# Kernel optimization log

Measured on AMD Instinct MI355X. Metric: run time of the kernel, lower is better.

## Reference

```python
import jax, jax.numpy as jnp
import numpy as np

EPS = 1e-5

def _layernorm(x, w, b):
    mu = jnp.mean(x, axis=-1, keepdims=True)
    var = jnp.mean((x - mu) ** 2, axis=-1, keepdims=True)
    return (x - mu) * jax.lax.rsqrt(var + EPS) * w + b

def _ssm(x, in_proj_w, x_proj_w, dt_proj_w, dt_proj_b, conv1d_w, conv1d_b,
         A_log, D, out_proj_w, norm_w, norm_b, d_state=16):
    # x: (B, L, d_model)
    xz = jnp.einsum('bld,ed->ble', x, in_proj_w)          # (B,L,2*d_inner)
    d_inner = xz.shape[-1] // 2
    x_in, z = xz[..., :d_inner], xz[..., d_inner:]
    # depthwise conv1d, kernel 3, pad 1
    xc = jax.lax.conv_general_dilated(
        jnp.transpose(x_in, (0, 2, 1)), conv1d_w,
        window_strides=(1,), padding=((1, 1),),
        feature_group_count=d_inner,
        dimension_numbers=('NCH', 'OIH', 'NCH'))
    xc = jnp.transpose(xc, (0, 2, 1)) + conv1d_b          # (B,L,d_inner)
    xc = jax.nn.silu(xc)
    dbc = jnp.einsum('bld,ed->ble', xc, x_proj_w)         # (B,L,1+2*d_state)
    delta = dbc[..., :1]
    B_mat = dbc[..., 1:1 + d_state]
    C_mat = dbc[..., 1 + d_state:]
    delta = jax.nn.softplus(jnp.einsum('blo,eo->ble', delta, dt_proj_w) + dt_proj_b)  # (B,L,d_inner)
    A = -jnp.exp(A_log)                                   # (d_inner,d_state)
    dA = jnp.exp(delta[..., None] * A[None, None])        # (B,L,d_inner,d_state)
    xbu = delta[..., None] * B_mat[:, :, None, :] * xc[..., None]
    def combine(c1, c2):
        a1, b1 = c1
        a2, b2 = c2
        return (a2 * a1, b2 + a2 * b1)
    _, h = jax.lax.associative_scan(combine, (dA, xbu), axis=1)  # h_t = dA_t h_{t-1} + xbu_t, h_0=0
    y = jnp.sum(h * C_mat[:, :, None, :], axis=-1)        # (B,L,d_inner)
    y = y + xc * D
    y = y * jax.nn.silu(z)
    y = _layernorm(y, norm_w, norm_b)
    return jnp.einsum('ble,de->bld', y, out_proj_w)

def reference(x, in_proj_w, x_proj_w, dt_proj_w, dt_proj_b, conv1d_w, conv1d_b,
              A_log, D, out_proj_w, norm_ssm_w, norm_ssm_b, norm1_w, norm1_b,
              dw_w, dw_b, gate):
    B, C, H, W = x.shape
    # local branch: depthwise 7x7 conv
    local = jax.lax.conv_general_dilated(
        x, dw_w, window_strides=(1, 1), padding=((3, 3), (3, 3)),
        feature_group_count=C, dimension_numbers=('NCHW', 'OIHW', 'NCHW'))
    local = local + dw_b[None, :, None, None]
    L = H * W
    max_seq_len = 256
    if L <= max_seq_len:
        x_flat = jnp.transpose(x, (0, 2, 3, 1)).reshape(B, L, C)
        ssm_out = _ssm(_layernorm(x_flat, norm1_w, norm1_b), in_proj_w, x_proj_w,
                       dt_proj_w, dt_proj_b, conv1d_w, conv1d_b, A_log, D,
                       out_proj_w, norm_ssm_w, norm_ssm_b)
        ssm_out = jnp.transpose(ssm_out.reshape(B, H, W, C), (0, 3, 1, 2))
    else:
        scale = (max_seq_len / L) ** 0.5
        h_s = max(1, int(H * scale))
        w_s = max(1, int(W * scale))
        # adaptive avg pool; H,W chosen divisible by h_s,w_s -> exact block mean
        x_small = x.reshape(B, C, h_s, H // h_s, w_s, W // w_s).mean(axis=(3, 5))
        x_flat = jnp.transpose(x_small, (0, 2, 3, 1)).reshape(B, h_s * w_s, C)
        ssm_small = _ssm(_layernorm(x_flat, norm1_w, norm1_b), in_proj_w, x_proj_w,
                         dt_proj_w, dt_proj_b, conv1d_w, conv1d_b, A_log, D,
                         out_proj_w, norm_ssm_w, norm_ssm_b)
        ssm_small = jnp.transpose(ssm_small.reshape(B, h_s, w_s, C), (0, 3, 1, 2))
        ssm_out = jax.image.resize(ssm_small, (B, C, H, W), method='bilinear')  # align_corners=False
    g = jax.nn.sigmoid(gate[0])
    return x + g * ssm_out + (1.0 - g) * local

def setup_inputs() -> dict:
    key = jax.random.key(0)
    ks = jax.random.split(key, 8)
    C, d_state, d_inner = 192, 16, 384
    Bsz, H, W = 32, 64, 64
    s = 0.02
    A = jnp.broadcast_to(jnp.arange(1, d_state + 1, dtype=jnp.float32), (d_inner, d_state))
    return {
        'x': jax.random.normal(ks[0], (Bsz, C, H, W), jnp.float32),
        'in_proj_w': jax.random.normal(ks[1], (2 * d_inner, C), jnp.float32) * s,
        'x_proj_w': jax.random.normal(ks[2], (2 * d_state + 1, d_inner), jnp.float32) * s,
        'dt_proj_w': jax.random.normal(ks[3], (d_inner, 1), jnp.float32) * s,
        'dt_proj_b': jnp.zeros((d_inner,), jnp.float32),
        'conv1d_w': jax.random.normal(ks[4], (d_inner, 1, 3), jnp.float32) * 0.2,
        'conv1d_b': jnp.zeros((d_inner,), jnp.float32),
        'A_log': jnp.log(A),
        'D': jnp.ones((d_inner,), jnp.float32),
        'out_proj_w': jax.random.normal(ks[5], (C, d_inner), jnp.float32) * s,
        'norm_ssm_w': jnp.ones((d_inner,), jnp.float32),
        'norm_ssm_b': jnp.zeros((d_inner,), jnp.float32),
        'norm1_w': jnp.ones((C,), jnp.float32),
        'norm1_b': jnp.zeros((C,), jnp.float32),
        'dw_w': jax.random.normal(ks[6], (C, 1, 7, 7), jnp.float32) * 0.05,
        'dw_b': jnp.zeros((C,), jnp.float32),
        'gate': jnp.ones((1,), jnp.float32),
    }
```

## Files before the change

kernel.cpp:

```cpp
#include <hip/hip_runtime.h>
#include <stdint.h>

#define B_   32
#define C_   192
#define Hh   64
#define Ww   64
#define LS   256
#define DI   384
#define DSt  16
#define E2   768

__global__ __launch_bounds__(256) void k_pool_ln(
    const float* __restrict__ x, const float* __restrict__ w, const float* __restrict__ bb,
    float* __restrict__ xln)
{
  int b = blockIdx.x >> 4, i = blockIdx.x & 15;
  int tid = threadIdx.x;
  int wv = tid >> 6;
  int off = tid & 63;
  int j = off & 15;

  __shared__ float pooledT[16 * 193];
  __shared__ float red1[4][16], red2[4][16];
  __shared__ float muL[16], rsL[16];

  const float* xbase = x + (((size_t)(b * C_) * Hh + i * 4) * Ww);
#pragma unroll 4
  for (int cc = 0; cc < 48; ++cc) {
    int c = cc * 4 + wv;
    float4 v = *reinterpret_cast<const float4*>(xbase + (size_t)c * (Hh * Ww) + off * 4);
    float s = v.x + v.y + v.z + v.w;
    s += __shfl_xor(s, 16, 64);
    s += __shfl_xor(s, 32, 64);
    if (off < 16) pooledT[j * 193 + c] = s * (1.f / 16.f);
  }
  __syncthreads();

  int j2 = tid & 15, cg = tid >> 4;
  float s1 = 0.f, s2 = 0.f;
#pragma unroll
  for (int ccx = 0; ccx < 12; ++ccx) {
    float v = pooledT[j2 * 193 + cg * 12 + ccx];
    s1 += v; s2 += v * v;
  }
  s1 += __shfl_xor(s1, 16, 64); s1 += __shfl_xor(s1, 32, 64);
  s2 += __shfl_xor(s2, 16, 64); s2 += __shfl_xor(s2, 32, 64);
  if ((tid & 63) < 16) { red1[tid >> 6][j2] = s1; red2[tid >> 6][j2] = s2; }
  __syncthreads();
  if (tid < 16) {
    float t1 = red1[0][tid] + red1[1][tid] + red1[2][tid] + red1[3][tid];
    float t2 = red2[0][tid] + red2[1][tid] + red2[2][tid] + red2[3][tid];
    float mu = t1 / 192.f;
    float var = t2 / 192.f - mu * mu;
    muL[tid] = mu; rsL[tid] = rsqrtf(var + 1e-5f);
  }
  __syncthreads();

#pragma unroll
  for (int k = 0; k < 12; ++k) {
    int o = tid + 256 * k;
    int c = o % 192, jj = o / 192;
    float v = (pooledT[jj * 193 + c] - muL[jj]) * rsL[jj] * w[c] + bb[c];
    xln[((size_t)(b * 256 + i * 16 + jj)) * C_ + c] = v;
  }
}

__global__ __launch_bounds__(256) void k_gemm_f32(
    const float* __restrict__ A, const float* __restrict__ W,
    float* __restrict__ C, int N, int K)
{
  __shared__ float At[8][132];
  __shared__ float Wt[8][132];
  int tid = threadIdx.x;
  int m0 = blockIdx.y * 128, n0 = blockIdx.x * 128;
  int tx = tid & 15, ty = tid >> 4;
  int lr = tid >> 1, lk = (tid & 1) * 4;
  float acc[8][8] = {};
  const float* Arow = A + (size_t)(m0 + lr) * K + lk;
  int wrow = n0 + lr; if (wrow >= N) wrow = N - 1;
  const float* Wrow = W + (size_t)wrow * K + lk;
  for (int k0 = 0; k0 < K; k0 += 8) {
    float4 av = *reinterpret_cast<const float4*>(Arow + k0);
    float4 wv = *reinterpret_cast<const float4*>(Wrow + k0);
    __syncthreads();
    At[lk + 0][lr] = av.x; At[lk + 1][lr] = av.y; At[lk + 2][lr] = av.z; At[lk + 3][lr] = av.w;
    Wt[lk + 0][lr] = wv.x; Wt[lk + 1][lr] = wv.y; Wt[lk + 2][lr] = wv.z; Wt[lk + 3][lr] = wv.w;
    __syncthreads();
#pragma unroll
    for (int k = 0; k < 8; ++k) {
      float4 a0 = *reinterpret_cast<const float4*>(&At[k][8 * ty]);
      float4 a1 = *reinterpret_cast<const float4*>(&At[k][8 * ty + 4]);
      float4 w0 = *reinterpret_cast<const float4*>(&Wt[k][8 * tx]);
      float4 w1 = *reinterpret_cast<const float4*>(&Wt[k][8 * tx + 4]);
      float a[8] = {a0.x, a0.y, a0.z, a0.w, a1.x, a1.y, a1.z, a1.w};
      float w[8] = {w0.x, w0.y, w0.z, w0.w, w1.x, w1.y, w1.z, w1.w};
#pragma unroll
      for (int i = 0; i < 8; ++i)
#pragma unroll
        for (int j = 0; j < 8; ++j) acc[i][j] += a[i] * w[j];
    }
  }
#pragma unroll
  for (int i = 0; i < 8; ++i) {
    int row = m0 + 8 * ty + i;
    int col0 = n0 + 8 * tx;
    if (col0 < N)
      *reinterpret_cast<float4*>(C + (size_t)row * N + col0) =
          make_float4(acc[i][0], acc[i][1], acc[i][2], acc[i][3]);
    if (col0 + 4 < N)
      *reinterpret_cast<float4*>(C + (size_t)row * N + col0 + 4) =
          make_float4(acc[i][4], acc[i][5], acc[i][6], acc[i][7]);
  }
}

__global__ __launch_bounds__(256) void k_conv_silu(
    const float* __restrict__ xz, const float* __restrict__ cw, const float* __restrict__ cb,
    float* __restrict__ xc)
{
  int idx = blockIdx.x * 256 + threadIdx.x;
  int e = idx % DI;
  int row = idx / DI;
  int l = row & 255;
  const float* xin = xz + (size_t)row * E2 + e;
  float x0 = *xin;
  float xm = (l > 0)   ? *(xin - E2) : 0.f;
  float xp = (l < 255) ? *(xin + E2) : 0.f;
  float v = cw[e * 3 + 0] * xm + cw[e * 3 + 1] * x0 + cw[e * 3 + 2] * xp + cb[e];
  xc[idx] = v / (1.f + expf(-v));
}

__global__ __launch_bounds__(256) void k_xproj(
    const float* __restrict__ xc, const float* __restrict__ xw,
    const float* __restrict__ dtw, const float* __restrict__ dtb,
    float* __restrict__ BC, float* __restrict__ delta)
{
  int wid = threadIdx.x >> 6, lane = threadIdx.x & 63;
  int row = blockIdx.x * 4 + wid;
  const float* xr = xc + (size_t)row * DI;
  float xv[6];
#pragma unroll
  for (int k = 0; k < 6; ++k) xv[k] = xr[lane + 64 * k];
  float dres = 0.f, mine = 0.f;
  for (int j = 0; j < 33; ++j) {
    const float* wr = xw + (size_t)j * DI;
    float p = 0.f;
#pragma unroll
    for (int k = 0; k < 6; ++k) p += wr[lane + 64 * k] * xv[k];
#pragma unroll
    for (int off = 32; off; off >>= 1) p += __shfl_xor(p, off, 64);
    if (j == 0) dres = p;
    else if (lane == j - 1) mine = p;
  }
  if (lane < 32) BC[(size_t)row * 32 + lane] = mine;
#pragma unroll
  for (int k = 0; k < 6; ++k) {
    int e = lane + 64 * k;
    float dr = dres * dtw[e] + dtb[e];
    delta[(size_t)row * DI + e] = dr > 20.f ? dr : log1pf(expf(dr));
  }
}

__global__ __launch_bounds__(256) void k_scan(
    const float* __restrict__ delta, const float* __restrict__ xc,
    const float* __restrict__ BC, const float* __restrict__ xz,
    const float* __restrict__ A_log, const float* __restrict__ Dp,
    float* __restrict__ yg)
{
  int blk = blockIdx.x;
  int b = blk / 24, eg = blk - b * 24;
  int tid = threadIdx.x;
  int et = tid >> 4, s = tid & 15;
  int e = eg * 16 + et;
  float Aes = -expf(A_log[e * DSt + s]);
  float Dv16 = Dp[e] * (1.f / 16.f);

  const float* dbase  = delta + (size_t)b * 256 * DI;
  const float* xbase  = xc    + (size_t)b * 256 * DI;
  const float* bcbase = BC    + (size_t)b * 256 * 32;
  const float* zbase  = xz    + (size_t)b * 256 * E2 + DI;
  float*       ybase  = yg    + (size_t)b * 256 * DI;

  __shared__ float tr[16 * 16 * 20];
  float* myw = &tr[(et * 16) * 20 + s];
  const float* myr = &tr[(et * 16 + s) * 20];

  float h = 0.f;
  for (int g = 0; g < 16; ++g) {
    int l0 = g * 16;
    float dv[16], xv[16], Bm[16], Cm[16];
#pragma unroll
    for (int i = 0; i < 16; ++i) {
      int row = l0 + i;
      dv[i] = dbase[row * DI + e];
      xv[i] = xbase[row * DI + e];
      Bm[i] = bcbase[row * 32 + s];
      Cm[i] = bcbase[row * 32 + 16 + s];
    }
    __syncthreads();
#pragma unroll
    for (int i = 0; i < 16; ++i) {
      float da = __expf(dv[i] * Aes);
      h = da * h + dv[i] * Bm[i] * xv[i];
      myw[i * 20] = h * Cm[i] + xv[i] * Dv16;
    }
    __syncthreads();
    float4 p0 = *reinterpret_cast<const float4*>(myr + 0);
    float4 p1 = *reinterpret_cast<const float4*>(myr + 4);
    float4 p2 = *reinterpret_cast<const float4*>(myr + 8);
    float4 p3 = *reinterpret_cast<const float4*>(myr + 12);
    float S = ((p0.x + p0.y) + (p0.z + p0.w)) + ((p1.x + p1.y) + (p1.z + p1.w))
            + ((p2.x + p2.y) + (p2.z + p2.w)) + ((p3.x + p3.y) + (p3.z + p3.w));
    int l = l0 + s;
    float zv = zbase[l * E2 + e];
    float y = S * (zv / (1.f + __expf(-zv)));
    ybase[l * DI + e] = y;
  }
}

__global__ __launch_bounds__(128) void k_ln_ssm(
    const float* __restrict__ yg, const float* __restrict__ nw, const float* __restrict__ nb,
    float* __restrict__ yn)
{
  int row = blockIdx.x;
  int t = threadIdx.x;
  const float* yr = yg + (size_t)row * DI;
  float v0 = yr[t], v1 = yr[t + 128], v2 = yr[t + 256];
  float s1 = v0 + v1 + v2, s2 = v0 * v0 + v1 * v1 + v2 * v2;
#pragma unroll
  for (int off = 32; off; off >>= 1) {
    s1 += __shfl_xor(s1, off, 64);
    s2 += __shfl_xor(s2, off, 64);
  }
  __shared__ float a1[2], a2[2];
  if ((t & 63) == 0) { a1[t >> 6] = s1; a2[t >> 6] = s2; }
  __syncthreads();
  float t1 = a1[0] + a1[1], t2 = a2[0] + a2[1];
  float mu = t1 / 384.f, var = t2 / 384.f - mu * mu;
  float rstd = rsqrtf(var + 1e-5f);
  float* yo = yn + (size_t)row * DI;
  yo[t]       = (v0 - mu) * rstd * nw[t]       + nb[t];
  yo[t + 128] = (v1 - mu) * rstd * nw[t + 128] + nb[t + 128];
  yo[t + 256] = (v2 - mu) * rstd * nw[t + 256] + nb[t + 256];
}

__global__ __launch_bounds__(256) void k_final(
    const float* __restrict__ x, const float* __restrict__ dww, const float* __restrict__ dwb,
    const float* __restrict__ ssm, const float* __restrict__ gate,
    float* __restrict__ out)
{
  int blk = blockIdx.x;
  int ti = blk & 3;
  int c = (blk >> 2) % C_;
  int b = blk / (4 * C_);
  int h0 = ti * 16;
  __shared__ float xpatch[22 * 72];
  __shared__ float wlds[49];
  __shared__ float slds[6 * 16];
  __shared__ float biass;
  int tid = threadIdx.x;
  if (tid < 49) wlds[tid] = dww[(size_t)c * 49 + tid];
  if (tid == 49) biass = dwb[c];
  int ibase = (h0 >> 2) - 1;
  if (tid < 96) {
    int ii = ibase + (tid >> 4);
    ii = ii < 0 ? 0 : (ii > 15 ? 15 : ii);
    int jj = tid & 15;
    slds[tid] = ssm[((size_t)(b * LS) + ii * 16 + jj) * C_ + c];
  }
  const float* xb = x + ((size_t)(b * C_ + c) * Hh) * Ww;
  for (int idx = tid; idx < 22 * 70; idx += 256) {
    int r = idx / 70, col = idx % 70;
    int gh = h0 - 3 + r, gw = col - 3;
    float v = 0.f;
    if (gh >= 0 && gh < 64 && gw >= 0 && gw < 64)
      v = xb[gh * 64 + gw];
    xpatch[r * 72 + col] = v;
  }
  __syncthreads();
  float g = 1.f / (1.f + expf(-gate[0]));
  int qn = tid >> 5;
  int R0 = qn * 2;
  int w0 = (tid & 31) * 2;
  float a00 = 0, a01 = 0, a10 = 0, a11 = 0;
#pragma unroll
  for (int k = 0; k < 8; ++k) {
    const float* prow = &xpatch[(R0 + k) * 72 + w0];
    float v[8];
#pragma unroll
    for (int d = 0; d < 8; ++d) v[d] = prow[d];
    if (k < 7) {
#pragma unroll
      for (int dx = 0; dx < 7; ++dx) {
        float wv = wlds[k * 7 + dx];
        a00 += wv * v[dx]; a01 += wv * v[dx + 1];
      }
    }
    if (k > 0) {
#pragma unroll
      for (int dx = 0; dx < 7; ++dx) {
        float wv = wlds[(k - 1) * 7 + dx];
        a10 += wv * v[dx]; a11 += wv * v[dx + 1];
      }
    }
  }
  float locs[2][2] = {{a00 + biass, a01 + biass}, {a10 + biass, a11 + biass}};
  float* orow = out + ((size_t)(b * C_ + c) * Hh) * Ww;
#pragma unroll
  for (int rr = 0; rr < 2; ++rr) {
    int hgl = h0 + R0 + rr;
    float ci = hgl * 0.25f - 0.375f;
    float fif = floorf(ci);
    int i0 = (int)fif;
    float fi = ci - fif;
    int li = i0 - ibase;
    const float* r0p = &slds[li * 16];
    const float* r1p = &slds[(li + 1) * 16];
    float ov[2];
#pragma unroll
    for (int ccx = 0; ccx < 2; ++ccx) {
      int wgl = w0 + ccx;
      float cj = wgl * 0.25f - 0.375f;
      float fjf = floorf(cj);
      int j0 = (int)fjf;
      float fj = cj - fjf;
      int jc0 = j0 < 0 ? 0 : j0;
      int jc1 = (j0 + 1) > 15 ? 15 : (j0 + 1);
      float sv = (1.f - fi) * ((1.f - fj) * r0p[jc0] + fj * r0p[jc1])
               +         fi * ((1.f - fj) * r1p[jc0] + fj * r1p[jc1]);
      float xv = xpatch[(R0 + rr + 3) * 72 + (wgl + 3)];
      ov[ccx] = xv + g * sv + (1.f - g) * locs[rr][ccx];
    }
    *reinterpret_cast<float2*>(&orow[hgl * 64 + w0]) = make_float2(ov[0], ov[1]);
  }
}

extern "C" void kernel_launch(void* const* d_in, const int* in_sizes, int n_in,
                              void* d_out, int out_size, void* d_ws, size_t ws_size,
                              hipStream_t stream)
{
  const float* x    = (const float*)d_in[0];
  const float* inw  = (const float*)d_in[1];
  const float* xw   = (const float*)d_in[2];
  const float* dtw  = (const float*)d_in[3];
  const float* dtb  = (const float*)d_in[4];
  const float* cw   = (const float*)d_in[5];
  const float* cb   = (const float*)d_in[6];
  const float* alog = (const float*)d_in[7];
  const float* Dp   = (const float*)d_in[8];
  const float* ow   = (const float*)d_in[9];
  const float* nsw  = (const float*)d_in[10];
  const float* nsb  = (const float*)d_in[11];
  const float* n1w  = (const float*)d_in[12];
  const float* n1b  = (const float*)d_in[13];
  const float* dww  = (const float*)d_in[14];
  const float* dwb  = (const float*)d_in[15];
  const float* gate = (const float*)d_in[16];

  char* ws = (char*)d_ws;
  float* xln   = (float*)ws; ws += (size_t)8192 * 192 * 4;
  float* xz    = (float*)ws; ws += (size_t)8192 * 768 * 4;
  float* xc    = (float*)ws; ws += (size_t)8192 * 384 * 4;
  float* delta = (float*)ws; ws += (size_t)8192 * 384 * 4;
  float* BC    = (float*)ws; ws += (size_t)8192 * 32 * 4;
  float* yg    = (float*)ws; ws += (size_t)8192 * 384 * 4;
  float* yn  = xz;
  float* ssm = xln;

  k_pool_ln<<<B_ * 16, 256, 0, stream>>>(x, n1w, n1b, xln);
  k_gemm_f32<<<dim3(6, 64), 256, 0, stream>>>(xln, inw, xz, 768, 192);
  k_conv_silu<<<12288, 256, 0, stream>>>(xz, cw, cb, xc);
  k_xproj<<<2048, 256, 0, stream>>>(xc, xw, dtw, dtb, BC, delta);
  k_scan<<<B_ * 24, 256, 0, stream>>>(delta, xc, BC, xz, alog, Dp, yg);
  k_ln_ssm<<<8192, 128, 0, stream>>>(yg, nsw, nsb, yn);
  k_gemm_f32<<<dim3(2, 64), 256, 0, stream>>>(yn, ow, ssm, 192, 384);
  k_final<<<24576, 256, 0, stream>>>(x, dww, dwb, ssm, gate, (float*)d_out);
}
```

Before: 477.7 us.

## Process whole 64x64 plane per block in final depthwise conv kernel

The final fused kernel now handles one full (batch, channel) plane per block instead of a quarter. It loads the padded input with float4 accesses into shared memory, and each thread computes a 4x4 output tile with the 7x7 weights held in registers. The bilinear upsample is rewritten with precomputed fractional weights (0.125/0.375/0.625/0.875) from a 3x3 neighbourhood. The aim is to cut halo reloads and per-pixel index math and to raise register reuse, at the cost of more shared memory, higher register pressure and fewer blocks.

```diff
diff --git a/kernel.cpp b/kernel.cpp
--- a/kernel.cpp
+++ b/kernel.cpp
@@ -249,88 +249,89 @@
     float* __restrict__ out)
 {
   int blk = blockIdx.x;
-  int ti = blk & 3;
-  int c = (blk >> 2) % C_;
-  int b = blk / (4 * C_);
-  int h0 = ti * 16;
-  __shared__ float xpatch[22 * 72];
-  __shared__ float wlds[49];
-  __shared__ float slds[6 * 16];
-  __shared__ float biass;
+  int c = blk % C_;
+  int b = blk / C_;
   int tid = threadIdx.x;
-  if (tid < 49) wlds[tid] = dww[(size_t)c * 49 + tid];
-  if (tid == 49) biass = dwb[c];
-  int ibase = (h0 >> 2) - 1;
-  if (tid < 96) {
-    int ii = ibase + (tid >> 4);
-    ii = ii < 0 ? 0 : (ii > 15 ? 15 : ii);
-    int jj = tid & 15;
-    slds[tid] = ssm[((size_t)(b * LS) + ii * 16 + jj) * C_ + c];
-  }
+  int ty = tid >> 4, tx = tid & 15;
+
+  __shared__ float xpad[70 * 72];
+  __shared__ float sld[256];
+
+  for (int i4 = tid; i4 < 1260; i4 += 256)
+    *reinterpret_cast<float4*>(&xpad[i4 * 4]) = make_float4(0.f, 0.f, 0.f, 0.f);
+  sld[tid] = ssm[((size_t)(b * LS) + tid) * C_ + c];
+  __syncthreads();
+
   const float* xb = x + ((size_t)(b * C_ + c) * Hh) * Ww;
-  for (int idx = tid; idx < 22 * 70; idx += 256) {
-    int r = idx / 70, col = idx % 70;
-    int gh = h0 - 3 + r, gw = col - 3;
-    float v = 0.f;
-    if (gh >= 0 && gh < 64 && gw >= 0 && gw < 64)
-      v = xb[gh * 64 + gw];
-    xpatch[r * 72 + col] = v;
-  }
-  __syncthreads();
-  float g = 1.f / (1.f + expf(-gate[0]));
-  int qn = tid >> 5;
-  int R0 = qn * 2;
-  int w0 = (tid & 31) * 2;
-  float a00 = 0, a01 = 0, a10 = 0, a11 = 0;
-#pragma unroll
-  for (int k = 0; k < 8; ++k) {
-    const float* prow = &xpatch[(R0 + k) * 72 + w0];
-    float v[8];
-#pragma unroll
-    for (int d = 0; d < 8; ++d) v[d] = prow[d];
-    if (k < 7) {
+#pragma unroll
+  for (int k = 0; k < 4; ++k) {
+    int idx = tid + 256 * k;
+    int row = idx >> 4, colq = idx & 15;
+    float4 v = *reinterpret_cast<const float4*>(xb + row * 64 + colq * 4);
+    *reinterpret_cast<float4*>(&xpad[(row + 3) * 72 + 4 + colq * 4]) = v;
+  }
+
+  float wr[49];
+#pragma unroll
+  for (int k = 0; k < 49; ++k) wr[k] = dww[(size_t)c * 49 + k];
+  float bias = dwb[c];
+  float g = 1.f / (1.f + __expf(-gate[0]));
+  __syncthreads();
+
+  float acc[4][4] = {};
+  const float* rowbase = &xpad[(4 * ty) * 72 + 4 * tx];
+#pragma unroll
+  for (int rr = 0; rr < 10; ++rr) {
+    float4 v0 = *reinterpret_cast<const float4*>(rowbase + rr * 72);
+    float4 v1 = *reinterpret_cast<const float4*>(rowbase + rr * 72 + 4);
+    float4 v2 = *reinterpret_cast<const float4*>(rowbase + rr * 72 + 8);
+    float v[12] = {v0.x, v0.y, v0.z, v0.w, v1.x, v1.y, v1.z, v1.w, v2.x, v2.y, v2.z, v2.w};
+#pragma unroll
+    for (int i = 0; i < 4; ++i) {
+      if (rr - i < 0 || rr - i > 6) continue;
+      int dy = rr - i;
 #pragma unroll
       for (int dx = 0; dx < 7; ++dx) {
-        float wv = wlds[k * 7 + dx];
-        a00 += wv * v[dx]; a01 += wv * v[dx + 1];
+        float wv = wr[dy * 7 + dx];
+#pragma unroll
+        for (int j = 0; j < 4; ++j)
+          acc[i][j] += wv * v[j + dx + 1];
       }
     }
-    if (k > 0) {
-#pragma unroll
-      for (int dx = 0; dx < 7; ++dx) {
-        float wv = wlds[(k - 1) * 7 + dx];
-        a10 += wv * v[dx]; a11 += wv * v[dx + 1];
-      }
-    }
-  }
-  float locs[2][2] = {{a00 + biass, a01 + biass}, {a10 + biass, a11 + biass}};
+  }
+
+  int rA = ty - 1 < 0 ? 0 : ty - 1;
+  int rC = ty + 1 > 15 ? 15 : ty + 1;
+  int cA = tx - 1 < 0 ? 0 : tx - 1;
+  int cC = tx + 1 > 15 ? 15 : tx + 1;
+  float sA0 = sld[rA * 16 + cA], sA1 = sld[rA * 16 + tx], sA2 = sld[rA * 16 + cC];
+  float sB0 = sld[ty * 16 + cA], sB1 = sld[ty * 16 + tx], sB2 = sld[ty * 16 + cC];
+  float sC0 = sld[rC * 16 + cA], sC1 = sld[rC * 16 + tx], sC2 = sld[rC * 16 + cC];
+  float hA[4] = {0.375f * sA0 + 0.625f * sA1, 0.125f * sA0 + 0.875f * sA1,
+                 0.875f * sA1 + 0.125f * sA2, 0.625f * sA1 + 0.375f * sA2};
+  float hB[4] = {0.375f * sB0 + 0.625f * sB1, 0.125f * sB0 + 0.875f * sB1,
+                 0.875f * sB1 + 0.125f * sB2, 0.625f * sB1 + 0.375f * sB2};
+  float hC[4] = {0.375f * sC0 + 0.625f * sC1, 0.125f * sC0 + 0.875f * sC1,
+                 0.875f * sC1 + 0.125f * sC2, 0.625f * sC1 + 0.375f * sC2};
+  float viA[4] = {0.375f, 0.125f, 0.f, 0.f};
+  float viB[4] = {0.625f, 0.875f, 0.875f, 0.625f};
+  float viC[4] = {0.f, 0.f, 0.125f, 0.375f};
+
+  float gm1 = 1.f - g;
   float* orow = out + ((size_t)(b * C_ + c) * Hh) * Ww;
 #pragma unroll
-  for (int rr = 0; rr < 2; ++rr) {
-    int hgl = h0 + R0 + rr;
-    float ci = hgl * 0.25f - 0.375f;
-    float fif = floorf(ci);
-    int i0 = (int)fif;
-    float fi = ci - fif;
-    int li = i0 - ibase;
-    const float* r0p = &slds[li * 16];
-    const float* r1p = &slds[(li + 1) * 16];
-    float ov[2];
-#pragma unroll
-    for (int ccx = 0; ccx < 2; ++ccx) {
-      int wgl = w0 + ccx;
-      float cj = wgl * 0.25f - 0.375f;
-      float fjf = floorf(cj);
-      int j0 = (int)fjf;
-      float fj = cj - fjf;
-      int jc0 = j0 < 0 ? 0 : j0;
-      int jc1 = (j0 + 1) > 15 ? 15 : (j0 + 1);
-      float sv = (1.f - fi) * ((1.f - fj) * r0p[jc0] + fj * r0p[jc1])
-               +         fi * ((1.f - fj) * r1p[jc0] + fj * r1p[jc1]);
-      float xv = xpatch[(R0 + rr + 3) * 72 + (wgl + 3)];
-      ov[ccx] = xv + g * sv + (1.f - g) * locs[rr][ccx];
-    }
-    *reinterpret_cast<float2*>(&orow[hgl * 64 + w0]) = make_float2(ov[0], ov[1]);
+  for (int i = 0; i < 4; ++i) {
+    int R = 4 * ty + i;
+    float4 xv = *reinterpret_cast<const float4*>(&xpad[(R + 3) * 72 + 4 + 4 * tx]);
+    float xvv[4] = {xv.x, xv.y, xv.z, xv.w};
+    float ov[4];
+#pragma unroll
+    for (int j = 0; j < 4; ++j) {
+      float sv = viA[i] * hA[j] + viB[i] * hB[j] + viC[i] * hC[j];
+      ov[j] = xvv[j] + g * sv + gm1 * (acc[i][j] + bias);
+    }
+    *reinterpret_cast<float4*>(&orow[R * 64 + 4 * tx]) =
+        make_float4(ov[0], ov[1], ov[2], ov[3]);
   }
 }
 
@@ -373,5 +374,5 @@
   k_scan<<<B_ * 24, 256, 0, stream>>>(delta, xc, BC, xz, alog, Dp, yg);
   k_ln_ssm<<<8192, 128, 0, stream>>>(yg, nsw, nsb, yn);
   k_gemm_f32<<<dim3(2, 64), 256, 0, stream>>>(yn, ow, ssm, 192, 384);
-  k_final<<<24576, 256, 0, stream>>>(x, dww, dwb, ssm, gate, (float*)d_out);
-}
+  k_final<<<B_ * C_, 256, 0, stream>>>(x, dww, dwb, ssm, gate, (float*)d_out);
+}
```

Measured after the change: 449.5 us. 5.9% less time.
